# Optimization experiments

Measured on AMD Instinct MI355X. Metric: run time of the kernel, lower is better.

## Reference

```python
import jax, jax.numpy as jnp
import numpy as np


def sign_ste(x):
    # torch BNN Binarize: sign() applied to .data => forward sign, backward identity (STE)
    return x + jax.lax.stop_gradient(jnp.sign(x) - x)


def setup_inputs() -> dict:
    key = jax.random.key(0)
    ks = jax.random.split(key, 5)
    B = 65536
    return {
        "x": jax.random.normal(ks[0], (B, 1, 28, 28), dtype=jnp.float32),
        "w_conv": jax.random.normal(ks[1], (3, 1, 4, 4), dtype=jnp.float32) * 0.1,
        "b_conv": jax.random.normal(ks[2], (3,), dtype=jnp.float32) * 0.1,
        "w_fc": jax.random.normal(ks[3], (10, 1875), dtype=jnp.float32) * 0.05,
        "b_fc": jax.random.normal(ks[4], (10,), dtype=jnp.float32) * 0.05,
    }


def reference(x, w_conv, b_conv, w_fc, b_fc):
    # BinarizeConv2d(1,3,4): binarize input (in_ch=1 != 3) and weights, float bias
    xb = sign_ste(x)
    wcb = sign_ste(w_conv)
    y = jax.lax.conv_general_dilated(
        xb, wcb, window_strides=(1, 1), padding="VALID",
        dimension_numbers=("NCHW", "OIHW", "NCHW"))  # [B,3,25,25]
    y = y + b_conv[None, :, None, None]
    h = y.reshape(y.shape[0], -1)  # [B,1875]
    # BinarizeLinear(1875,10): binarize input (1875 != 784) and weights
    hb = sign_ste(h)
    wfb = sign_ste(w_fc)
    out = hb @ wfb.T + b_fc  # [B,10]
    return sign_ste(out)
```

## Files before the change

kernel.cpp:

```cpp
#include <hip/hip_runtime.h>
#include <stdint.h>

#define IMB 64
#define NBLK (65536 / IMB)

__device__ __forceinline__ void FA(uint32_t a, uint32_t b, uint32_t c,
                                   uint32_t& s, uint32_t& cy) {
  uint32_t ab = a ^ b;
  s = ab ^ c;
  cy = (a & b) | (ab & c);
}

__global__ __launch_bounds__(256) void bnn_fused(
    const float* __restrict__ x, const float* __restrict__ w_conv,
    const float* __restrict__ b_conv, const float* __restrict__ w_fc,
    const float* __restrict__ b_fc, float* __restrict__ out)
{
  __shared__ uint8_t  nib[IMB * 196];
  __shared__ uint32_t srows[IMB * 29];
  __shared__ __align__(16) uint32_t swf[900];
  const int tid = threadIdx.x;

  uint32_t wm[3][16], sbc[3];
#pragma unroll
  for (int c = 0; c < 3; ++c) {
#pragma unroll
    for (int uv = 0; uv < 16; ++uv)
      wm[c][uv] = (uint32_t)((int32_t)__float_as_uint(w_conv[c * 16 + uv]) >> 31);
    sbc[c] = (uint32_t)((int32_t)__float_as_uint(b_conv[c]) >> 31);
  }

  for (int s = tid; s < 750; s += 256) {
    int ci = s / 10, k = s - ci * 10;
    const float* wr = w_fc + k * 1875 + ci * 25;
    uint32_t m = 0;
#pragma unroll
    for (int j = 0; j < 25; ++j)
      m |= (__float_as_uint(wr[j]) >> 31) << j;
    swf[ci * 12 + k] = m;
  }

  const float4* xv = (const float4*)(x + (size_t)blockIdx.x * (IMB * 784));
#pragma unroll 4
  for (int q = 0; q < 49; ++q) {
    int idx = q * 256 + tid;
    float4 v = xv[idx];
    uint32_t n = (__float_as_uint(v.x) >> 31)
               | ((__float_as_uint(v.y) >> 31) << 1)
               | ((__float_as_uint(v.z) >> 31) << 2)
               | ((__float_as_uint(v.w) >> 31) << 3);
    nib[idx] = (uint8_t)n;
  }
  __syncthreads();

#pragma unroll
  for (int q = 0; q < 7; ++q) {
    int r = q * 256 + tid;
    const uint8_t* p = &nib[r * 7];
    uint32_t m = (uint32_t)p[0]        | ((uint32_t)p[1] << 4)
               | ((uint32_t)p[2] << 8) | ((uint32_t)p[3] << 12)
               | ((uint32_t)p[4] << 16)| ((uint32_t)p[5] << 20)
               | ((uint32_t)p[6] << 24);
    int mi = r / 28, rowin = r - mi * 28;
    srows[mi * 29 + rowin] = m;
  }
  __syncthreads();

  const int sub = tid & 3;
  const int img = tid >> 2;
  const uint32_t* my = &srows[img * 29];
  int nd[10] = {0,0,0,0,0,0,0,0,0,0};
  int ilo = sub * 7;
  int ihi = ilo + 7; if (ihi > 25) ihi = 25;

  for (int i = ilo; i < ihi; ++i) {
    uint32_t r0 = my[i], r1 = my[i + 1], r2 = my[i + 2], r3 = my[i + 3];
#pragma unroll
    for (int c = 0; c < 3; ++c) {
      const uint32_t* W = wm[c];
      uint32_t s0, c0, s1, c1, s2, c2, s3, c3, s4, c4;
      FA( r0 ^ W[0],        (r0 ^ W[1])  >> 1, (r0 ^ W[2])  >> 2, s0, c0);
      FA((r0 ^ W[3]) >> 3,   r1 ^ W[4],        (r1 ^ W[5])  >> 1, s1, c1);
      FA((r1 ^ W[6]) >> 2,  (r1 ^ W[7])  >> 3,  r2 ^ W[8],        s2, c2);
      FA((r2 ^ W[9]) >> 1,  (r2 ^ W[10]) >> 2, (r2 ^ W[11]) >> 3, s3, c3);
      FA( r3 ^ W[12],       (r3 ^ W[13]) >> 1, (r3 ^ W[14]) >> 2, s4, c4);
      uint32_t t15 = (r3 ^ W[15]) >> 3;
      uint32_t u0, d0, u1, d1;
      FA(s0, s1, s2, u0, d0); FA(s3, s4, t15, u1, d1);
      uint32_t bb0 = u0 ^ u1, e0 = u0 & u1;
      uint32_t p0, q0, p1, q1, p2, q2;
      FA(c0, c1, c2, p0, q0); FA(c3, c4, d0, p1, q1); FA(d1, e0, p0, p2, q2);
      uint32_t bb1 = p1 ^ p2, q3 = p1 & p2;
      uint32_t r0_, r1_;
      FA(q0, q1, q2, r0_, r1_);
      uint32_t bb2 = r0_ ^ q3, r2_ = r0_ & q3;
      uint32_t bb3 = r1_ ^ r2_, bb4 = r1_ & r2_;
      uint32_t low = bb0 | bb1 | bb2;
      uint32_t neg = (bb4 | (bb3 & (low | sbc[c]))) & 0x1FFFFFFu;
      int ci = c * 25 + i;
      uint4 wA = *(const uint4*)&swf[ci * 12];
      uint4 wB = *(const uint4*)&swf[ci * 12 + 4];
      uint2 wC = *(const uint2*)&swf[ci * 12 + 8];
      nd[0] += __popc(neg ^ wA.x); nd[1] += __popc(neg ^ wA.y);
      nd[2] += __popc(neg ^ wA.z); nd[3] += __popc(neg ^ wA.w);
      nd[4] += __popc(neg ^ wB.x); nd[5] += __popc(neg ^ wB.y);
      nd[6] += __popc(neg ^ wB.z); nd[7] += __popc(neg ^ wB.w);
      nd[8] += __popc(neg ^ wC.x); nd[9] += __popc(neg ^ wC.y);
    }
  }

#pragma unroll
  for (int k = 0; k < 10; ++k) nd[k] += __shfl_xor(nd[k], 1);
#pragma unroll
  for (int k = 0; k < 10; ++k) nd[k] += __shfl_xor(nd[k], 2);

  if (sub == 0) {
    const size_t bi = (size_t)blockIdx.x * IMB + img;
    float* op = out + bi * 10;
#pragma unroll
    for (int k = 0; k < 10; k += 2) {
      float v0 = (float)(1875 - 2 * nd[k])     + b_fc[k];
      float v1 = (float)(1875 - 2 * nd[k + 1]) + b_fc[k + 1];
      float2 st;
      st.x = v0 < 0.f ? -1.f : (v0 > 0.f ? 1.f : 0.f);
      st.y = v1 < 0.f ? -1.f : (v1 > 0.f ? 1.f : 0.f);
      *(float2*)(op + k) = st;
    }
  }
}

extern "C" void kernel_launch(void* const* d_in, const int* in_sizes, int n_in,
                              void* d_out, int out_size, void* d_ws, size_t ws_size,
                              hipStream_t stream) {
  const float* x      = (const float*)d_in[0];
  const float* w_conv = (const float*)d_in[1];
  const float* b_conv = (const float*)d_in[2];
  const float* w_fc   = (const float*)d_in[3];
  const float* b_fc   = (const float*)d_in[4];
  bnn_fused<<<NBLK, 256, 0, stream>>>(x, w_conv, b_conv, w_fc, b_fc,
                                      (float*)d_out);
}
```

Baseline: 303.4 us.

## Stream input via global_load_lds double-buffered per-wave chunks into row bitmasks

Replaces the register float4 load, nibble packing and second LDS repack pass with per-wave double-buffered async global-to-LDS copies (global_load_lds, 16 bytes per lane). Each lane then builds a full 28-bit row mask straight from the raw LDS floats, and vmcnt waits overlap the next chunk's load with packing of the current one. Launch bounds now request two blocks per CU. The raw staging buffer is about 57 KB of LDS, which may limit occupancy, and correctness depends on the hand-written vmcnt accounting.

Measured after the change: 293.4 us. 1.03x faster.

```diff
diff --git a/kernel.cpp b/kernel.cpp
--- a/kernel.cpp
+++ b/kernel.cpp
@@ -3,6 +3,20 @@
 
 #define IMB 64
 #define NBLK (65536 / IMB)
+#define CHUNK_B 7168
+#define NCHUNK 28
+
+__device__ __forceinline__ void gload16(const void* g, void* l) {
+  __builtin_amdgcn_global_load_lds(
+      (const __attribute__((address_space(1))) uint32_t*)g,
+      (__attribute__((address_space(3))) uint32_t*)l, 16, 0, 0);
+}
+
+#define VMWAIT(N)                                                  \
+  do {                                                             \
+    asm volatile("s_waitcnt vmcnt(" #N ")" ::: "memory");          \
+    __builtin_amdgcn_sched_barrier(0);                             \
+  } while (0)
 
 __device__ __forceinline__ void FA(uint32_t a, uint32_t b, uint32_t c,
                                    uint32_t& s, uint32_t& cy) {
@@ -11,15 +25,41 @@
   cy = (a & b) | (ab & c);
 }
 
-__global__ __launch_bounds__(256) void bnn_fused(
+__device__ __forceinline__ void issue_chunk(const uint8_t* gsrc, uint8_t* slot,
+                                            int c, int lane) {
+  const uint8_t* s = gsrc + (size_t)c * CHUNK_B + lane * 16;
+  uint8_t* d = slot + lane * 16;
+#pragma unroll
+  for (int i = 0; i < 7; ++i) gload16(s + i * 1024, d + i * 1024);
+}
+
+__device__ __forceinline__ void proc_chunk(const uint8_t* slot, int c, int lane,
+                                           uint32_t* srows) {
+  const uint8_t* rp = slot + lane * 112;
+  uint32_t m = 0;
+#pragma unroll
+  for (int q = 0; q < 7; ++q) {
+    uint4 v = *(const uint4*)(rp + q * 16);
+    uint32_t n = (v.x >> 31) | ((v.y >> 31) << 1) | ((v.z >> 31) << 2) |
+                 ((v.w >> 31) << 3);
+    m |= n << (4 * q);
+  }
+  uint32_t g = (uint32_t)c * 64u + (uint32_t)lane;
+  uint32_t img = g / 28u;
+  uint32_t rowin = g - img * 28u;
+  srows[img * 29 + rowin] = m;
+}
+
+__global__ __launch_bounds__(256, 2) void bnn_fused(
     const float* __restrict__ x, const float* __restrict__ w_conv,
     const float* __restrict__ b_conv, const float* __restrict__ w_fc,
     const float* __restrict__ b_fc, float* __restrict__ out)
 {
-  __shared__ uint8_t  nib[IMB * 196];
+  __shared__ __align__(16) uint8_t  raw[4 * 2 * CHUNK_B];
   __shared__ uint32_t srows[IMB * 29];
   __shared__ __align__(16) uint32_t swf[900];
   const int tid = threadIdx.x;
+  const int w = tid >> 6, lane = tid & 63;
 
   uint32_t wm[3][16], sbc[3];
 #pragma unroll
@@ -40,30 +80,28 @@
     swf[ci * 12 + k] = m;
   }
 
-  const float4* xv = (const float4*)(x + (size_t)blockIdx.x * (IMB * 784));
-#pragma unroll 4
-  for (int q = 0; q < 49; ++q) {
-    int idx = q * 256 + tid;
-    float4 v = xv[idx];
-    uint32_t n = (__float_as_uint(v.x) >> 31)
-               | ((__float_as_uint(v.y) >> 31) << 1)
-               | ((__float_as_uint(v.z) >> 31) << 2)
-               | ((__float_as_uint(v.w) >> 31) << 3);
-    nib[idx] = (uint8_t)n;
-  }
-  __syncthreads();
+  asm volatile("s_waitcnt vmcnt(0)" ::: "memory");
+  __builtin_amdgcn_sched_barrier(0);
 
-#pragma unroll
-  for (int q = 0; q < 7; ++q) {
-    int r = q * 256 + tid;
-    const uint8_t* p = &nib[r * 7];
-    uint32_t m = (uint32_t)p[0]        | ((uint32_t)p[1] << 4)
-               | ((uint32_t)p[2] << 8) | ((uint32_t)p[3] << 12)
-               | ((uint32_t)p[4] << 16)| ((uint32_t)p[5] << 20)
-               | ((uint32_t)p[6] << 24);
-    int mi = r / 28, rowin = r - mi * 28;
-    srows[mi * 29 + rowin] = m;
-  }
+  const uint8_t* gsrc = (const uint8_t*)(x + (size_t)blockIdx.x * (IMB * 784));
+  uint8_t* slot0 = &raw[(w * 2 + 0) * CHUNK_B];
+  uint8_t* slot1 = &raw[(w * 2 + 1) * CHUNK_B];
+
+  issue_chunk(gsrc, slot0, w + 4 * 0, lane);
+  issue_chunk(gsrc, slot1, w + 4 * 1, lane);
+  VMWAIT(7); proc_chunk(slot0, w + 4 * 0, lane, srows);
+  issue_chunk(gsrc, slot0, w + 4 * 2, lane);
+  VMWAIT(7); proc_chunk(slot1, w + 4 * 1, lane, srows);
+  issue_chunk(gsrc, slot1, w + 4 * 3, lane);
+  VMWAIT(7); proc_chunk(slot0, w + 4 * 2, lane, srows);
+  issue_chunk(gsrc, slot0, w + 4 * 4, lane);
+  VMWAIT(7); proc_chunk(slot1, w + 4 * 3, lane, srows);
+  issue_chunk(gsrc, slot1, w + 4 * 5, lane);
+  VMWAIT(7); proc_chunk(slot0, w + 4 * 4, lane, srows);
+  issue_chunk(gsrc, slot0, w + 4 * 6, lane);
+  VMWAIT(7); proc_chunk(slot1, w + 4 * 5, lane, srows);
+  VMWAIT(0); proc_chunk(slot0, w + 4 * 6, lane, srows);
+
   __syncthreads();
 
   const int sub = tid & 3;
```
